# Optimization experiments

Measured on AMD Instinct MI355X. Metric: run time of the kernel, lower is better.

The kernel has to match this reference:

```python
import jax, jax.numpy as jnp
import numpy as np


def setup_inputs() -> dict:
    key = jax.random.key(0)
    ks = jax.random.split(key, 9)
    B, D_IN, UNITS, TOPICS, VOCAB = 64, 512, 1024, 20, 32000
    return {
        "inputs": jax.random.normal(ks[0], (B, D_IN), jnp.float32),
        "prev_state": jax.random.normal(ks[1], (B, UNITS), jnp.float32),
        "kernel": jax.random.normal(ks[2], (D_IN, UNITS), jnp.float32) * 0.02,
        "recurrent_kernel": jax.random.normal(ks[3], (UNITS, UNITS), jnp.float32) * 0.02,
        "bernoli_kernel": jax.random.normal(ks[4], (UNITS, 1), jnp.float32) * 0.02,
        "vocab_kernel": jax.random.normal(ks[5], (UNITS, VOCAB), jnp.float32) * 0.02,
        "beta": jax.random.normal(ks[6], (TOPICS, VOCAB), jnp.float32),
        "indicators": jax.random.randint(ks[7], (B,), 0, 2, jnp.int32),
        "indices": jax.random.randint(ks[8], (B,), 0, VOCAB, jnp.int32),
    }


def reference(inputs, prev_state, kernel, recurrent_kernel, bernoli_kernel,
              vocab_kernel, beta, indicators, indices):
    # h_t = x @ W_xh + h_{t-1} @ W_hh   -> [B, units]
    next_state = inputs @ kernel + prev_state @ recurrent_kernel
    # stop-word Bernoulli prob: sigmoid(softplus(h_t @ w_b))  -> [B, 1]
    bern_p = jax.nn.sigmoid(jax.nn.softplus(next_state @ bernoli_kernel))
    bern_p = bern_p[..., None]  # [B, 1, 1]
    # deterministic sampling key (reference baseline)
    samp_key = jax.random.key(42)
    bern_samples = jax.random.bernoulli(samp_key, bern_p).astype(jnp.float32)
    # logits: [B,1,V] + (1 - l_t) * beta[T,V] -> [B, T, V]
    logits = (next_state @ vocab_kernel)[:, None, :] + (1.0 - bern_samples) * beta
    word_prob_out = jax.nn.softmax(logits, axis=-1)
    return word_prob_out, next_state
```

## Files before the change

kernel.cpp:

```cpp
#include <hip/hip_runtime.h>
#include <cstdint>
#include <cstddef>

typedef unsigned int u32;
typedef unsigned short u16;

#define NB 64
#define DIN 512
#define UNITS 1024
#define TOPICS 20
#define VOCAB 32000
#define NS_OFF ((size_t)NB * TOPICS * VOCAB)

__device__ __forceinline__ float bf2f(u16 h) {
    union { u32 u; float f; } c; c.u = ((u32)h) << 16; return c.f;
}
__device__ __forceinline__ u16 f2bf(float f) {
    union { float f; u32 u; } c; c.f = f;
    u32 r = c.u + 0x7FFFu + ((c.u >> 16) & 1u);
    return (u16)(r >> 16);
}
template<bool F32>
__device__ __forceinline__ float ldv(const void* p, size_t i) {
    if constexpr (F32) return ((const float*)p)[i];
    else return bf2f(((const u16*)p)[i]);
}
__device__ __forceinline__ float ldr(const void* p, size_t i, bool f32) {
    return f32 ? ((const float*)p)[i] : bf2f(((const u16*)p)[i]);
}

__device__ __forceinline__ u32 threefry_bits_partitionable(u32 i) {
    const u32 ks0 = 0u, ks1 = 42u, ks2 = 0u ^ 42u ^ 0x1BD11BDAu;
    u32 x0 = 0u + ks0, x1 = i + ks1;
#define TF_R(r) { x0 += x1; x1 = (x1 << r) | (x1 >> (32 - r)); x1 ^= x0; }
    TF_R(13) TF_R(15) TF_R(26) TF_R(6)
    x0 += ks1; x1 += ks2 + 1u;
    TF_R(17) TF_R(29) TF_R(16) TF_R(24)
    x0 += ks2; x1 += ks0 + 2u;
    TF_R(13) TF_R(15) TF_R(26) TF_R(6)
    x0 += ks0; x1 += ks1 + 3u;
    TF_R(17) TF_R(29) TF_R(16) TF_R(24)
    x0 += ks1; x1 += ks2 + 4u;
    TF_R(13) TF_R(15) TF_R(26) TF_R(6)
    x0 += ks2; x1 += ks0 + 5u;
#undef TF_R
    return x0 ^ x1;
}

__global__ __launch_bounds__(256)
void k_init(const void* __restrict__ beta, int* __restrict__ flag,
            float* __restrict__ lsum, float* __restrict__ eb) {
    int tid = threadIdx.x, lane = tid & 63, w = tid >> 6;
    __shared__ int cnt_s[4];
    int cnt = 0;
    const u32* braw = (const u32*)beta;
    for (int i = tid; i < 1024; i += 256) {
        u32 x = braw[i];
        u32 e = (x >> 7) & 0xFFu;
        cnt += (e >= 110u && e <= 132u) ? 1 : 0;
    }
    for (int off = 32; off; off >>= 1) cnt += __shfl_down(cnt, off, 64);
    if (lane == 0) cnt_s[w] = cnt;
    __syncthreads();
    int total = cnt_s[0] + cnt_s[1] + cnt_s[2] + cnt_s[3];
    bool f32 = total < 512;

    size_t base = (size_t)blockIdx.x * 2000;
    for (int i = tid; i < 2000; i += 256)
        eb[base + i] = __expf(ldr(beta, base + i, f32));

    if (blockIdx.x == 0) {
        for (int i = tid; i < NB * TOPICS; i += 256) lsum[i] = 0.f;
        if (tid == 0) flag[0] = f32 ? 1 : 0;
    }
}

template<bool F32>
__device__ void state_body(const void* xin, const void* h0, const void* Wxh,
                           const void* Whh, float* ns_f32, void* dout) {
    __shared__ float lx[DIN + UNITS];
    int b = blockIdx.x >> 2;
    int u = ((blockIdx.x & 3) << 8) | threadIdx.x;
    for (int i = threadIdx.x; i < DIN; i += 256)
        lx[i] = ldv<F32>(xin, (size_t)b * DIN + i);
    for (int i = threadIdx.x; i < UNITS; i += 256)
        lx[DIN + i] = ldv<F32>(h0, (size_t)b * UNITS + i);
    __syncthreads();
    float acc = 0.f;
#pragma unroll 8
    for (int k = 0; k < DIN; ++k)   acc += lx[k]       * ldv<F32>(Wxh, (size_t)k * UNITS + u);
#pragma unroll 8
    for (int k = 0; k < UNITS; ++k) acc += lx[DIN + k] * ldv<F32>(Whh, (size_t)k * UNITS + u);
    int idx = b * UNITS + u;
    ns_f32[idx] = acc;
    if constexpr (F32) ((float*)dout)[NS_OFF + idx] = acc;
    else               ((u16*)dout)[NS_OFF + idx]   = f2bf(acc);
}
__global__ __launch_bounds__(256)
void k_state(const int* __restrict__ flag, const void* xin, const void* h0,
             const void* Wxh, const void* Whh,
             float* __restrict__ ns_f32, void* dout) {
    if (*flag) state_body<true>(xin, h0, Wxh, Whh, ns_f32, dout);
    else       state_body<false>(xin, h0, Wxh, Whh, ns_f32, dout);
}

template<bool F32>
__device__ void bern_body(const float* ns, const void* bk, float* coeff) {
    int b = blockIdx.x, lane = threadIdx.x;
    float s = 0.f;
#pragma unroll
    for (int i = 0; i < UNITS / 64; ++i) {
        int k = lane + (i << 6);
        s += ns[b * UNITS + k] * ldv<F32>(bk, k);
    }
    for (int off = 32; off; off >>= 1) s += __shfl_down(s, off, 64);
    if (lane == 0) {
        float sp = log1pf(expf(s));
        float p  = 1.f / (1.f + expf(-sp));
        u32 bits = threefry_bits_partitionable((u32)b);
        union { u32 u; float f; } c; c.u = (bits >> 9) | 0x3f800000u;
        float uni = c.f - 1.0f;
        coeff[b] = (uni < p) ? 0.f : 1.f;
    }
}
__global__ __launch_bounds__(64)
void k_bern(const int* __restrict__ flag, const float* __restrict__ ns,
            const void* bk, float* __restrict__ coeff) {
    if (*flag) bern_body<true>(ns, bk, coeff);
    else       bern_body<false>(ns, bk, coeff);
}

#define SV_KT 64
#define SV_AP 68
#define SV_BP 192
template<bool F32>
__device__ void sv_body(const float* __restrict__ ns, const void* __restrict__ Wv,
                        float* __restrict__ esv) {
    __shared__ float As[SV_KT * SV_AP];
    __shared__ float Bs[SV_KT * SV_BP];
    const int tid = threadIdx.x;
    const int tb = tid >> 4;
    const int tv = tid & 15;
    const int v0 = blockIdx.x * 128;

    const int sa_b = tid >> 1;
    const int sa_k = (tid & 1) * 32;

    float4  aR[8];
    float4  bR[16];
    ushort4 bRh[16];

    float acc[8][8];
#pragma unroll
    for (int r = 0; r < 8; ++r)
#pragma unroll
        for (int c = 0; c < 8; ++c) acc[r][c] = 0.f;

#pragma unroll
    for (int j = 0; j < 8; ++j)
        aR[j] = *(const float4*)&ns[(size_t)sa_b * UNITS + sa_k + j * 4];
#pragma unroll
    for (int i = 0; i < 16; ++i) {
        int e = tid + i * 128, row = e >> 5, c4 = e & 31;
        if constexpr (F32)
            bR[i] = *(const float4*)((const float*)Wv + (size_t)row * VOCAB + v0 + c4 * 4);
        else
            bRh[i] = *(const ushort4*)((const u16*)Wv + (size_t)row * VOCAB + v0 + c4 * 4);
    }

    for (int t = 0; t < 16; ++t) {
#pragma unroll
        for (int j = 0; j < 8; ++j) {
            int kl = sa_k + j * 4;
            As[(kl + 0) * SV_AP + sa_b] = aR[j].x;
            As[(kl + 1) * SV_AP + sa_b] = aR[j].y;
            As[(kl + 2) * SV_AP + sa_b] = aR[j].z;
            As[(kl + 3) * SV_AP + sa_b] = aR[j].w;
        }
#pragma unroll
        for (int i = 0; i < 16; ++i) {
            int e = tid + i * 128, row = e >> 5, c4 = e & 31;
            float4 w;
            if constexpr (F32) w = bR[i];
            else { w.x = bf2f(bRh[i].x); w.y = bf2f(bRh[i].y);
                   w.z = bf2f(bRh[i].z); w.w = bf2f(bRh[i].w); }
            *(float4*)&Bs[row * SV_BP + (c4 >> 1) * 12 + (c4 & 1) * 4] = w;
        }
        __syncthreads();

        if (t < 15) {
            int k0n = (t + 1) * SV_KT;
#pragma unroll
            for (int j = 0; j < 8; ++j)
                aR[j] = *(const float4*)&ns[(size_t)sa_b * UNITS + k0n + sa_k + j * 4];
#pragma unroll
            for (int i = 0; i < 16; ++i) {
                int e = tid + i * 128, row = e >> 5, c4 = e & 31;
                if constexpr (F32)
                    bR[i] = *(const float4*)((const float*)Wv + (size_t)(k0n + row) * VOCAB + v0 + c4 * 4);
                else
                    bRh[i] = *(const ushort4*)((const u16*)Wv + (size_t)(k0n + row) * VOCAB + v0 + c4 * 4);
            }
        }

#pragma unroll 8
        for (int kk = 0; kk < SV_KT; ++kk) {
            float4 a0 = *(const float4*)&As[kk * SV_AP + tb * 8];
            float4 a1 = *(const float4*)&As[kk * SV_AP + tb * 8 + 4];
            float4 b0 = *(const float4*)&Bs[kk * SV_BP + tv * 12];
            float4 b1 = *(const float4*)&Bs[kk * SV_BP + tv * 12 + 4];
            float av[8] = {a0.x, a0.y, a0.z, a0.w, a1.x, a1.y, a1.z, a1.w};
            float bv[8] = {b0.x, b0.y, b0.z, b0.w, b1.x, b1.y, b1.z, b1.w};
#pragma unroll
            for (int r = 0; r < 8; ++r)
#pragma unroll
                for (int c = 0; c < 8; ++c)
                    acc[r][c] = fmaf(av[r], bv[c], acc[r][c]);
        }
        __syncthreads();
    }

#pragma unroll
    for (int r = 0; r < 8; ++r) {
        float4 e0, e1;
        e0.x = __expf(acc[r][0]); e0.y = __expf(acc[r][1]);
        e0.z = __expf(acc[r][2]); e0.w = __expf(acc[r][3]);
        e1.x = __expf(acc[r][4]); e1.y = __expf(acc[r][5]);
        e1.z = __expf(acc[r][6]); e1.w = __expf(acc[r][7]);
        float* dst = esv + (size_t)(tb * 8 + r) * VOCAB + v0 + tv * 8;
        *(float4*)dst = e0;
        *(float4*)(dst + 4) = e1;
    }
}
__global__ __launch_bounds__(128)
void k_sv(const int* __restrict__ flag, const float* __restrict__ ns,
          const void* Wv, float* __restrict__ esv) {
    if (*flag) sv_body<true>(ns, Wv, esv);
    else       sv_body<false>(ns, Wv, esv);
}

__global__ __launch_bounds__(256)
void k_sum(const float* __restrict__ esv, const float* __restrict__ eb,
           const float* __restrict__ coeff, float* __restrict__ lsum) {
    int b = blockIdx.y, tid = threadIdx.x;
    float c = coeff[b];
    const float4* e4 = (const float4*)(esv + (size_t)b * VOCAB);
    int i0 = blockIdx.x * 256 + tid;
    __shared__ float red[4][TOPICS];
    int lane = tid & 63, w = tid >> 6;

    if (c != 0.f) {
        float acc[TOPICS];
#pragma unroll
        for (int t = 0; t < TOPICS; ++t) acc[t] = 0.f;
        for (int i = i0; i < VOCAB / 4; i += 4096) {
            float4 e = e4[i];
#pragma unroll
            for (int t = 0; t < TOPICS; ++t) {
                float4 g = *(const float4*)(eb + (size_t)t * VOCAB + i * 4);
                acc[t] += e.x * g.x + e.y * g.y + e.z * g.z + e.w * g.w;
            }
        }
#pragma unroll
        for (int t = 0; t < TOPICS; ++t) {
            float v = acc[t];
            for (int off = 32; off; off >>= 1) v += __shfl_down(v, off, 64);
            if (lane == 0) red[w][t] = v;
        }
        __syncthreads();
        if (tid < TOPICS) {
            float s = red[0][tid] + red[1][tid] + red[2][tid] + red[3][tid];
            atomicAdd(&lsum[b * TOPICS + tid], s);
        }
    } else {
        float a = 0.f;
        for (int i = i0; i < VOCAB / 4; i += 4096) {
            float4 e = e4[i];
            a += e.x + e.y + e.z + e.w;
        }
        for (int off = 32; off; off >>= 1) a += __shfl_down(a, off, 64);
        if (lane == 0) red[w][0] = a;
        __syncthreads();
        if (tid < TOPICS) {
            float s = red[0][0] + red[1][0] + red[2][0] + red[3][0];
            atomicAdd(&lsum[b * TOPICS + tid], s);
        }
    }
}

template<bool F32>
__device__ void write_body(const float* esv, const float* eb, const float* coeff,
                           const float* lsum, void* dout) {
    int b = blockIdx.y, tid = threadIdx.x;
    int v0 = blockIdx.x * 2048 + tid * 8;
    if (v0 >= VOCAB) return;
    float c = coeff[b];
    const float* er = esv + (size_t)b * VOCAB + v0;
    float4 e0 = *(const float4*)er;
    float4 e1 = *(const float4*)(er + 4);
#pragma unroll 4
    for (int t = 0; t < TOPICS; ++t) {
        float inv = 1.0f / lsum[b * TOPICS + t];
        float o0, o1, o2, o3, o4, o5, o6, o7;
        if (c != 0.f) {
            const float* gr = eb + (size_t)t * VOCAB + v0;
            float4 g0 = *(const float4*)gr;
            float4 g1 = *(const float4*)(gr + 4);
            o0 = e0.x * g0.x * inv; o1 = e0.y * g0.y * inv;
            o2 = e0.z * g0.z * inv; o3 = e0.w * g0.w * inv;
            o4 = e1.x * g1.x * inv; o5 = e1.y * g1.y * inv;
            o6 = e1.z * g1.z * inv; o7 = e1.w * g1.w * inv;
        } else {
            o0 = e0.x * inv; o1 = e0.y * inv; o2 = e0.z * inv; o3 = e0.w * inv;
            o4 = e1.x * inv; o5 = e1.y * inv; o6 = e1.z * inv; o7 = e1.w * inv;
        }
        size_t off = (size_t)b * TOPICS * VOCAB + (size_t)t * VOCAB + v0;
        if constexpr (F32) {
            float4 s0 = {o0, o1, o2, o3}, s1 = {o4, o5, o6, o7};
            *(float4*)((float*)dout + off) = s0;
            *(float4*)((float*)dout + off + 4) = s1;
        } else {
            uint4 st;
            st.x = (u32)f2bf(o0) | ((u32)f2bf(o1) << 16);
            st.y = (u32)f2bf(o2) | ((u32)f2bf(o3) << 16);
            st.z = (u32)f2bf(o4) | ((u32)f2bf(o5) << 16);
            st.w = (u32)f2bf(o6) | ((u32)f2bf(o7) << 16);
            *(uint4*)((u16*)dout + off) = st;
        }
    }
}
__global__ __launch_bounds__(256)
void k_write(const int* __restrict__ flag, const float* __restrict__ esv,
             const float* __restrict__ eb, const float* __restrict__ coeff,
             const float* __restrict__ lsum, void* dout) {
    if (*flag) write_body<true>(esv, eb, coeff, lsum, dout);
    else       write_body<false>(esv, eb, coeff, lsum, dout);
}

extern "C" void kernel_launch(void* const* d_in, const int* in_sizes, int n_in,
                              void* d_out, int out_size, void* d_ws, size_t ws_size,
                              hipStream_t stream) {
    const void* xin  = d_in[0];
    const void* h0   = d_in[1];
    const void* Wxh  = d_in[2];
    const void* Whh  = d_in[3];
    const void* bk   = d_in[4];
    const void* Wv   = d_in[5];
    const void* beta = d_in[6];

    char* ws = (char*)d_ws;
    int*   flag   = (int*)  (ws + 0);
    float* coeff  = (float*)(ws + 256);
    float* lsum   = (float*)(ws + 1024);
    float* ns_f32 = (float*)(ws + 8192);
    float* eb     = (float*)(ws + 270336);
    float* esv    = (float*)(ws + 2830336);

    k_init <<<320, 256, 0, stream>>>(beta, flag, lsum, eb);
    k_state<<<256, 256, 0, stream>>>(flag, xin, h0, Wxh, Whh, ns_f32, d_out);
    k_bern <<<64, 64, 0, stream>>>(flag, ns_f32, bk, coeff);
    k_sv   <<<250, 128, 0, stream>>>(flag, ns_f32, Wv, esv);
    k_sum  <<<dim3(16, 64), 256, 0, stream>>>(esv, eb, coeff, lsum);
    k_write<<<dim3(16, 64), 256, 0, stream>>>(flag, esv, eb, coeff, lsum, d_out);
}
```

Before: 497.0 us.

## Use bf16 MFMA for vocab projection GEMM with swizzled LDS and double buffering

Replaces the FP32 FMA tiled GEMM for the vocab logits with a bf16 MFMA 16x16x32 path. It reads the bf16 next_state from the output buffer and stages A in XOR-swizzled shared memory, double-buffered against register-prefetched B columns. The grid goes from 250 blocks of 128 threads to 500 blocks of 256. The FP32 path is rewritten as a simpler 64-wide tile. B loads are scalar strided 2-byte reads per lane, which could limit bandwidth, and the bf16 path relies on the output buffer already holding a bf16 copy of next_state.

```diff
diff --git a/kernel.cpp b/kernel.cpp
--- a/kernel.cpp
+++ b/kernel.cpp
@@ -11,6 +11,9 @@
 #define TOPICS 20
 #define VOCAB 32000
 #define NS_OFF ((size_t)NB * TOPICS * VOCAB)
+
+typedef __attribute__((ext_vector_type(8))) short s16x8;
+typedef __attribute__((ext_vector_type(4))) float f32x4;
 
 __device__ __forceinline__ float bf2f(u16 h) {
     union { u32 u; float f; } c; c.u = ((u32)h) << 16; return c.f;
@@ -130,113 +133,155 @@
     else       bern_body<false>(ns, bk, coeff);
 }
 
-#define SV_KT 64
-#define SV_AP 68
-#define SV_BP 192
-template<bool F32>
-__device__ void sv_body(const float* __restrict__ ns, const void* __restrict__ Wv,
-                        float* __restrict__ esv) {
-    __shared__ float As[SV_KT * SV_AP];
-    __shared__ float Bs[SV_KT * SV_BP];
-    const int tid = threadIdx.x;
-    const int tb = tid >> 4;
-    const int tv = tid & 15;
-    const int v0 = blockIdx.x * 128;
-
-    const int sa_b = tid >> 1;
-    const int sa_k = (tid & 1) * 32;
-
-    float4  aR[8];
-    float4  bR[16];
-    ushort4 bRh[16];
-
-    float acc[8][8];
-#pragma unroll
-    for (int r = 0; r < 8; ++r)
-#pragma unroll
-        for (int c = 0; c < 8; ++c) acc[r][c] = 0.f;
-
-#pragma unroll
-    for (int j = 0; j < 8; ++j)
-        aR[j] = *(const float4*)&ns[(size_t)sa_b * UNITS + sa_k + j * 4];
-#pragma unroll
-    for (int i = 0; i < 16; ++i) {
-        int e = tid + i * 128, row = e >> 5, c4 = e & 31;
-        if constexpr (F32)
-            bR[i] = *(const float4*)((const float*)Wv + (size_t)row * VOCAB + v0 + c4 * 4);
-        else
-            bRh[i] = *(const ushort4*)((const u16*)Wv + (size_t)row * VOCAB + v0 + c4 * 4);
-    }
-
-    for (int t = 0; t < 16; ++t) {
-#pragma unroll
-        for (int j = 0; j < 8; ++j) {
-            int kl = sa_k + j * 4;
-            As[(kl + 0) * SV_AP + sa_b] = aR[j].x;
-            As[(kl + 1) * SV_AP + sa_b] = aR[j].y;
-            As[(kl + 2) * SV_AP + sa_b] = aR[j].z;
-            As[(kl + 3) * SV_AP + sa_b] = aR[j].w;
-        }
-#pragma unroll
-        for (int i = 0; i < 16; ++i) {
-            int e = tid + i * 128, row = e >> 5, c4 = e & 31;
-            float4 w;
-            if constexpr (F32) w = bR[i];
-            else { w.x = bf2f(bRh[i].x); w.y = bf2f(bRh[i].y);
-                   w.z = bf2f(bRh[i].z); w.w = bf2f(bRh[i].w); }
-            *(float4*)&Bs[row * SV_BP + (c4 >> 1) * 12 + (c4 & 1) * 4] = w;
-        }
-        __syncthreads();
-
-        if (t < 15) {
-            int k0n = (t + 1) * SV_KT;
-#pragma unroll
-            for (int j = 0; j < 8; ++j)
-                aR[j] = *(const float4*)&ns[(size_t)sa_b * UNITS + k0n + sa_k + j * 4];
-#pragma unroll
-            for (int i = 0; i < 16; ++i) {
-                int e = tid + i * 128, row = e >> 5, c4 = e & 31;
-                if constexpr (F32)
-                    bR[i] = *(const float4*)((const float*)Wv + (size_t)(k0n + row) * VOCAB + v0 + c4 * 4);
-                else
-                    bRh[i] = *(const ushort4*)((const u16*)Wv + (size_t)(k0n + row) * VOCAB + v0 + c4 * 4);
+#define PAD 68
+#define SV_SMEM_BYTES (2 * 64 * PAD * 4)
+
+__device__ __forceinline__ void sv_mfma_body(const short* __restrict__ ns16,
+                                             const short* __restrict__ Wv,
+                                             float* __restrict__ esv,
+                                             char* smem_raw) {
+    short* As = (short*)smem_raw;
+    const int tid  = threadIdx.x;
+    const int lane = tid & 63;
+    const int wn   = tid >> 6;
+    const int v0   = blockIdx.x * 64;
+    const int col  = v0 + wn * 16 + (lane & 15);
+    const int krow = (lane >> 4) * 8;
+
+    const short* Bcol = Wv + col;
+
+    f32x4 acc[4];
+#pragma unroll
+    for (int m = 0; m < 4; ++m) acc[m] = (f32x4){0.f, 0.f, 0.f, 0.f};
+
+    short bA[16], bB[16];
+
+    auto loadB = [&](short* buf, int t) {
+#pragma unroll
+        for (int kf = 0; kf < 2; ++kf)
+#pragma unroll
+            for (int e = 0; e < 8; ++e)
+                buf[kf * 8 + e] = Bcol[(size_t)(t * 64 + kf * 32 + krow + e) * VOCAB];
+    };
+    auto stageA = [&](int dbase, int t) {
+#pragma unroll
+        for (int r = 0; r < 2; ++r) {
+            int e = tid + r * 256;
+            int row = e >> 3, c = e & 7;
+            s16x8 v = *(const s16x8*)&ns16[(size_t)row * UNITS + t * 64 + c * 8];
+            *(s16x8*)&As[dbase + row * 64 + ((c * 8) ^ ((row & 7) << 3))] = v;
+        }
+    };
+    auto compute = [&](int dbase, const short* buf) {
+        s16x8 aF[4][2];
+#pragma unroll
+        for (int mf = 0; mf < 4; ++mf)
+#pragma unroll
+            for (int kf = 0; kf < 2; ++kf) {
+                int row = mf * 16 + (lane & 15);
+                int co  = (kf * 32 + krow) ^ ((row & 7) << 3);
+                aF[mf][kf] = *(const s16x8*)&As[dbase + row * 64 + co];
             }
-        }
-
-#pragma unroll 8
-        for (int kk = 0; kk < SV_KT; ++kk) {
-            float4 a0 = *(const float4*)&As[kk * SV_AP + tb * 8];
-            float4 a1 = *(const float4*)&As[kk * SV_AP + tb * 8 + 4];
-            float4 b0 = *(const float4*)&Bs[kk * SV_BP + tv * 12];
-            float4 b1 = *(const float4*)&Bs[kk * SV_BP + tv * 12 + 4];
-            float av[8] = {a0.x, a0.y, a0.z, a0.w, a1.x, a1.y, a1.z, a1.w};
-            float bv[8] = {b0.x, b0.y, b0.z, b0.w, b1.x, b1.y, b1.z, b1.w};
-#pragma unroll
-            for (int r = 0; r < 8; ++r)
-#pragma unroll
-                for (int c = 0; c < 8; ++c)
-                    acc[r][c] = fmaf(av[r], bv[c], acc[r][c]);
-        }
-        __syncthreads();
-    }
-
-#pragma unroll
-    for (int r = 0; r < 8; ++r) {
+#pragma unroll
+        for (int kf = 0; kf < 2; ++kf) {
+            s16x8 bF;
+#pragma unroll
+            for (int e = 0; e < 8; ++e) bF[e] = buf[kf * 8 + e];
+#pragma unroll
+            for (int mf = 0; mf < 4; ++mf)
+                acc[mf] = __builtin_amdgcn_mfma_f32_16x16x32_bf16(
+                              aF[mf][kf], bF, acc[mf], 0, 0, 0);
+        }
+    };
+
+    loadB(bA, 0);
+    for (int t = 0; t < 16; t += 2) {
+        stageA(0, t);
+        __syncthreads();
+        loadB(bB, t + 1);
+        compute(0, bA);
+        stageA(64 * 64, t + 1);
+        __syncthreads();
+        if (t + 2 < 16) loadB(bA, t + 2);
+        compute(64 * 64, bB);
+    }
+
+#pragma unroll
+    for (int mf = 0; mf < 4; ++mf)
+#pragma unroll
+        for (int r = 0; r < 4; ++r) {
+            int b = mf * 16 + (lane >> 4) * 4 + r;
+            esv[(size_t)b * VOCAB + col] = __expf(acc[mf][r]);
+        }
+}
+
+__device__ void sv_f32_body(const float* __restrict__ ns, const float* __restrict__ Wv,
+                            float* __restrict__ esv, float* As, float* Bs) {
+    int tid = threadIdx.x;
+    int vt = tid & 7;
+    int bg = tid >> 3;
+    int v0 = blockIdx.x * 64;
+    float acc[2][8];
+#pragma unroll
+    for (int r = 0; r < 2; ++r)
+#pragma unroll
+        for (int j = 0; j < 8; ++j) acc[r][j] = 0.f;
+
+    for (int k0 = 0; k0 < UNITS; k0 += 64) {
+        __syncthreads();
+        for (int e = tid; e < 1024; e += 256) {
+            int row = e >> 4, c4 = e & 15;
+            *(float4*)&As[row * PAD + c4 * 4] =
+                *(const float4*)&ns[row * UNITS + k0 + c4 * 4];
+        }
+        for (int e = tid; e < 1024; e += 256) {
+            int row = e >> 4, c4 = e & 15;
+            *(float4*)&Bs[row * PAD + c4 * 4] =
+                *(const float4*)(Wv + (size_t)(k0 + row) * VOCAB + v0 + c4 * 4);
+        }
+        __syncthreads();
+#pragma unroll 4
+        for (int u = 0; u < 64; u += 4) {
+            float4 a0 = *(float4*)&As[(bg * 2 + 0) * PAD + u];
+            float4 a1 = *(float4*)&As[(bg * 2 + 1) * PAD + u];
+            float aa0[4] = {a0.x, a0.y, a0.z, a0.w};
+            float aa1[4] = {a1.x, a1.y, a1.z, a1.w};
+#pragma unroll
+            for (int uu = 0; uu < 4; ++uu) {
+                float4 b0 = *(float4*)&Bs[(u + uu) * PAD + vt * 8];
+                float4 b1 = *(float4*)&Bs[(u + uu) * PAD + vt * 8 + 4];
+                float bb[8] = {b0.x, b0.y, b0.z, b0.w, b1.x, b1.y, b1.z, b1.w};
+#pragma unroll
+                for (int j = 0; j < 8; ++j) {
+                    acc[0][j] = fmaf(aa0[uu], bb[j], acc[0][j]);
+                    acc[1][j] = fmaf(aa1[uu], bb[j], acc[1][j]);
+                }
+            }
+        }
+    }
+#pragma unroll
+    for (int r = 0; r < 2; ++r) {
         float4 e0, e1;
         e0.x = __expf(acc[r][0]); e0.y = __expf(acc[r][1]);
         e0.z = __expf(acc[r][2]); e0.w = __expf(acc[r][3]);
         e1.x = __expf(acc[r][4]); e1.y = __expf(acc[r][5]);
         e1.z = __expf(acc[r][6]); e1.w = __expf(acc[r][7]);
-        float* dst = esv + (size_t)(tb * 8 + r) * VOCAB + v0 + tv * 8;
+        float* dst = esv + (size_t)(bg * 2 + r) * VOCAB + v0 + vt * 8;
         *(float4*)dst = e0;
         *(float4*)(dst + 4) = e1;
     }
 }
-__global__ __launch_bounds__(128)
+
+__global__ __launch_bounds__(256)
 void k_sv(const int* __restrict__ flag, const float* __restrict__ ns,
-          const void* Wv, float* __restrict__ esv) {
-    if (*flag) sv_body<true>(ns, Wv, esv);
-    else       sv_body<false>(ns, Wv, esv);
+          const void* Wv, const void* dout, float* __restrict__ esv) {
+    __shared__ __align__(16) char smem[SV_SMEM_BYTES];
+    if (*flag) {
+        float* As = (float*)smem;
+        sv_f32_body(ns, (const float*)Wv, esv, As, As + 64 * PAD);
+    } else {
+        sv_mfma_body((const short*)dout + NS_OFF, (const short*)Wv, esv, smem);
+    }
 }
 
 __global__ __launch_bounds__(256)
@@ -359,7 +404,7 @@
     k_init <<<320, 256, 0, stream>>>(beta, flag, lsum, eb);
     k_state<<<256, 256, 0, stream>>>(flag, xin, h0, Wxh, Whh, ns_f32, d_out);
     k_bern <<<64, 64, 0, stream>>>(flag, ns_f32, bk, coeff);
-    k_sv   <<<250, 128, 0, stream>>>(flag, ns_f32, Wv, esv);
+    k_sv   <<<500, 256, 0, stream>>>(flag, ns_f32, Wv, d_out, esv);
     k_sum  <<<dim3(16, 64), 256, 0, stream>>>(esv, eb, coeff, lsum);
     k_write<<<dim3(16, 64), 256, 0, stream>>>(flag, esv, eb, coeff, lsum, d_out);
 }
```

New measurement: 482.6 us. 1.03x faster.
